# Optimization experiments

Measured on AMD Instinct MI355X. Metric: run time of the kernel, lower is better.

## Reference

```python
import jax, jax.numpy as jnp
import numpy as np

RADIUS = 2
K = 2 * RADIUS + 1          # kernel_size
NP = K ** 3                  # n_patches = 125
GAMMA_W = 3.3257199          # scipy.stats.t.ppf(1 - 0.005/2, df=8+8-2)
SIGMA_INV = jnp.array([0.1, 0.1, 0.1, 50., 50., 50., 10., 10., 10.], dtype=jnp.float32)


def _shift(x):
    """x: (C,H,W,T) -> (C, K^3, H, W, T): all neighbors within radius, zero-padded borders.
    Equivalent to Tile(pad=radius) + extract_patches_3ds(valid) + combine."""
    C, H, W, T = x.shape
    xp = jnp.pad(x, ((0, 0), (RADIUS, RADIUS), (RADIUS, RADIUS), (RADIUS, RADIUS)))
    sl = [xp[:, i:i + H, j:j + W, k:k + T]
          for i in range(K) for j in range(K) for k in range(K)]
    return jnp.stack(sl, axis=1)


def _compute_w(ei, ej, vi, vj):
    """Optimal weight w_ij (StatDenoiser.compute_w)."""
    d2 = (ei - ej) ** 2
    num = 2.0 * d2 + vi + vj
    den = 2.0 * (d2 + vi + vj)
    # den==0 implies num==0 (all terms nonneg) -> w = 0.5
    w = jnp.where(den == 0, 0.5, num / jnp.where(den == 0, 1.0, den))
    var_zero = (vi == 0) | (vj == 0)
    w = jnp.where(var_zero & (ei != ej), 1.0, w)
    return w


def _t_statistic(w):
    """t = sqrt(1/(2(1-w)) - 1), inf at w==1 (StatDenoiser.compute_t_statistic)."""
    w_safe = jnp.minimum(w, 1.0 - 1e-7)
    t = jnp.sqrt(jnp.maximum(1.0 / (2.0 * (1.0 - w_safe)) - 1.0, 0.0))
    return jnp.where(w >= 1.0, jnp.inf, t)


def setup_inputs() -> dict:
    key = jax.random.key(0)
    k1, k2, k3, k4 = jax.random.split(key, 4)
    noisy = jax.random.uniform(k1, (3, 128, 128, 4), dtype=jnp.float32)
    guidance = jax.random.normal(k2, (9, 128, 128, 4), dtype=jnp.float32)
    estimands = jax.random.uniform(k3, (3, 128, 128, 4), dtype=jnp.float32)
    estimands_variance = jax.random.uniform(k4, (3, 128, 128, 4), dtype=jnp.float32)
    return {"noisy": noisy, "guidance": guidance,
            "estimands": estimands, "estimands_variance": estimands_variance}


def reference(noisy, guidance, estimands, estimands_variance):
    # ---- bilateral weights from guidance (compute_bilateral_weights) ----
    sg = _shift(guidance)                                  # (9, P, H, W, T)
    diff2 = (sg - guidance[:, None]) ** 2                  # center patch == guidance itself
    bw = jnp.exp(-0.5 * jnp.einsum('c,cphwt->phwt', SIGMA_INV, diff2))  # (P,H,W,T)

    # ---- statistical membership (compute_membership) ----
    se = _shift(estimands)                                 # (3, P, H, W, T)
    sv = _shift(estimands_variance)
    ei = estimands[:, None]                                # center estimand
    vi = estimands_variance[:, None]
    w_ij = _compute_w(ei, se, vi, sv)                      # (3, P, H, W, T)
    t = _t_statistic(w_ij)
    membership = jnp.all(t <= GAMMA_W, axis=0).astype(noisy.dtype)      # (P,H,W,T)

    # ---- combine: normalized weighted average of neighbor radiance ----
    fw = bw * membership                                   # (P,H,W,T)
    sn = _shift(noisy)                                     # (3, P, H, W, T)
    out = jnp.einsum('phwt,cphwt->chwt', fw, sn) / jnp.maximum(fw.sum(axis=0), 1e-12)
    return out
```

## Files before the change

### kernel.cpp

```cpp
#include <hip/hip_runtime.h>

typedef float v2f __attribute__((ext_vector_type(2)));

namespace {

constexpr int H = 128, W = 128, NPIX = H * W;
constexpr double GAMMA_Wd = 3.3257199;
constexpr float GAM2 = (float)(GAMMA_Wd * GAMMA_Wd);
constexpr float VBIG  = 1e30f;
constexpr float NHUGE = -1e38f;

constexpr int TR = 4, TC = 16;
constexpr int HR = TR + 4, HC = TC + 4;
constexpr int NSITE = HR * HC;
constexpr int NK = 18;
constexpr int KP = 19;
constexpr int NTHR = 256;

constexpr double S2LOG2E = 1.2011224087864498;
constexpr float SCA0 = (float)(0.22360679774997896 * S2LOG2E);
constexpr float SCA1 = (float)(5.0                 * S2LOG2E);
constexpr float SCA2 = (float)(2.2360679774997896  * S2LOG2E);

__global__ __launch_bounds__(NTHR)
__attribute__((amdgpu_waves_per_eu(2, 8)))
void statden(const float4* __restrict__ noisy,
             const float4* __restrict__ guid,
             const float4* __restrict__ est,
             const float4* __restrict__ var,
             float4* __restrict__ out)
{
    __shared__ float4 halo[NSITE * KP];

    const int tid   = threadIdx.x;
    const int tiler = blockIdx.x >> 3;
    const int tilec = blockIdx.x & 7;
    const int r0 = tiler * TR - 2;
    const int c0 = tilec * TC - 2;

    for (int u = tid; u < NSITE * NK; u += NTHR) {
        const int k    = u / NSITE;
        const int site = u - k * NSITE;
        const int sr  = site / HC;
        const int scp = site - sr * HC;
        const int gr = r0 + sr;
        const int gc = c0 + scp;
        const bool varslot = (k >= 12) && (k < 15);
        float4 v;
        if (((unsigned)gr < (unsigned)H) && ((unsigned)gc < (unsigned)W)) {
            const int gpix = (gr << 7) + gc;
            if (k < 9) {
                const float sca = (k < 3) ? SCA0 : (k < 6) ? SCA1 : SCA2;
                const float4 g = guid[k * NPIX + gpix];
                v = make_float4(g.x * sca, g.y * sca, g.z * sca, g.w * sca);
            } else if (k < 12) {
                v = est[(k - 9) * NPIX + gpix];
            } else if (k < 15) {
                const float4 w4 = var[(k - 12) * NPIX + gpix];
                v.x = (w4.x == 0.f) ? -VBIG : GAM2 * w4.x;
                v.y = (w4.y == 0.f) ? -VBIG : GAM2 * w4.y;
                v.z = (w4.z == 0.f) ? -VBIG : GAM2 * w4.z;
                v.w = (w4.w == 0.f) ? -VBIG : GAM2 * w4.w;
            } else {
                v = noisy[(k - 15) * NPIX + gpix];
            }
        } else {
            const float pad = varslot ? -VBIG : 0.f;
            v = make_float4(pad, pad, pad, pad);
        }
        halo[site * KP + k] = v;
    }
    __syncthreads();

    const int p  = tid & 63;
    const int s  = tid >> 6;
    const int pr = p >> 4;
    const int pc = p & 15;

    const float4* cs = &halo[((pr + 2) * HC + (pc + 2)) * KP];

    v2f gcc[9][2];
    v2f nqc[2] = {{0.f, 0.f}, {0.f, 0.f}};
#pragma unroll
    for (int c = 0; c < 9; ++c) {
        const float4 g = cs[c];
        gcc[c][0] = (v2f){g.x, g.y};
        gcc[c][1] = (v2f){g.z, g.w};
        nqc[0] -= gcc[c][0] * gcc[c][0];
        nqc[1] -= gcc[c][1] * gcc[c][1];
    }
    v2f eiP[3][2], viP[3][2];
#pragma unroll
    for (int c = 0; c < 3; ++c) {
        const float4 e = cs[9 + c];
        eiP[c][0] = (v2f){e.x, e.y}; eiP[c][1] = (v2f){e.z, e.w};
        const float4 w4 = cs[12 + c];
        viP[c][0] = (v2f){w4.x, w4.y}; viP[c][1] = (v2f){w4.z, w4.w};
    }

    v2f accP[3][2] = {};
    v2f denP[2] = {};

#pragma unroll
    for (int cc = 0; cc < 7; ++cc) {
        const int col = (cc << 2) + s;
        if (col < 25) {
            const int di = col / 5 - 2;
            const int dj = col - (col / 5) * 5 - 2;
            const float4* js = &halo[((pr + 2 + di) * HC + (pc + 2 + dj)) * KP];

            v2f qj2[2] = {};
            v2f cr[4][2] = {};
#pragma unroll
            for (int c = 0; c < 9; ++c) {
                const float4 g = js[c];
                const v2f g01 = (v2f){g.x, g.y}, g23 = (v2f){g.z, g.w};
                qj2[0] += g01 * g01;  qj2[1] += g23 * g23;
                cr[0][0] += gcc[c][0] * g.x;  cr[0][1] += gcc[c][1] * g.x;
                cr[1][0] += gcc[c][0] * g.y;  cr[1][1] += gcc[c][1] * g.y;
                cr[2][0] += gcc[c][0] * g.z;  cr[2][1] += gcc[c][1] * g.z;
                cr[3][0] += gcc[c][0] * g.w;  cr[3][1] += gcc[c][1] * g.w;
            }

            v2f rm[4][2];
#pragma unroll
            for (int c = 0; c < 3; ++c) {
                const float4 e4 = js[9 + c];
                const float4 w4 = js[12 + c];
                const float ejs[4] = {e4.x, e4.y, e4.z, e4.w};
                const float vjs[4] = {w4.x, w4.y, w4.z, w4.w};
#pragma unroll
                for (int tt = 0; tt < 4; ++tt) {
#pragma unroll
                    for (int hf = 0; hf < 2; ++hf) {
                        const v2f d  = eiP[c][hf] - ejs[tt];
                        const v2f S  = viP[c][hf] + vjs[tt];
                        const v2f dd = d * d;
                        const v2f r  = S - dd;
                        const v2f z  = dd * NHUGE;
                        const v2f rf = __builtin_elementwise_max(r, z);
                        rm[tt][hf] = (c == 0) ? rf
                                   : __builtin_elementwise_min(rm[tt][hf], rf);
                    }
                }
            }

            v2f f01[4], f23[4];
#pragma unroll
            for (int tt = 0; tt < 4; ++tt) {
                const float qjt = qj2[tt >> 1][tt & 1];
                const v2f a0 = cr[tt][0] * 2.f + (nqc[0] - qjt);
                const v2f a1 = cr[tt][1] * 2.f + (nqc[1] - qjt);
                float fv[4];
#pragma unroll
                for (int t = 0; t < 4; ++t) {
                    const bool valid = (tt - t <= 2) && (t - tt <= 2);
                    if (valid) {
                        const float av = (t < 2) ? a0[t & 1] : a1[t & 1];
                        const float rv = (t < 2) ? rm[tt][0][t & 1] : rm[tt][1][t & 1];
                        const float e  = __builtin_exp2f(av);
                        fv[t] = (rv >= 0.f) ? e : 0.f;
                    } else {
                        fv[t] = 0.f;
                    }
                }
                f01[tt] = (v2f){fv[0], fv[1]};
                f23[tt] = (v2f){fv[2], fv[3]};
                denP[0] += f01[tt];
                denP[1] += f23[tt];
            }
#pragma unroll
            for (int c = 0; c < 3; ++c) {
                const float4 n4 = js[15 + c];
                const float njs[4] = {n4.x, n4.y, n4.z, n4.w};
#pragma unroll
                for (int tt = 0; tt < 4; ++tt) {
                    accP[c][0] += f01[tt] * njs[tt];
                    accP[c][1] += f23[tt] * njs[tt];
                }
            }
        }
    }

    __syncthreads();
    float* red = reinterpret_cast<float*>(halo);
    {
        float* r = red + (s * 64 + p) * 17;
#pragma unroll
        for (int c = 0; c < 3; ++c) {
            r[c * 4 + 0] = accP[c][0][0]; r[c * 4 + 1] = accP[c][0][1];
            r[c * 4 + 2] = accP[c][1][0]; r[c * 4 + 3] = accP[c][1][1];
        }
        r[12] = denP[0][0]; r[13] = denP[0][1];
        r[14] = denP[1][0]; r[15] = denP[1][1];
    }
    __syncthreads();

    if (tid < 64) {
        float v[16];
        const float* rp = red + p * 17;
#pragma unroll
        for (int i = 0; i < 16; ++i) v[i] = rp[i];
#pragma unroll
        for (int k = 1; k < 4; ++k) {
            const float* rk = red + (k * 64 + p) * 17;
#pragma unroll
            for (int i = 0; i < 16; ++i) v[i] += rk[i];
        }

        const float cnt[4] = {50.f, 25.f, 25.f, 50.f};
        const float qn[4]  = {nqc[0][0], nqc[0][1], nqc[1][0], nqc[1][1]};
        const float e0[4]  = {eiP[0][0][0], eiP[0][0][1], eiP[0][1][0], eiP[0][1][1]};
        const float e1[4]  = {eiP[1][0][0], eiP[1][0][1], eiP[1][1][0], eiP[1][1][1]};
        const float e2[4]  = {eiP[2][0][0], eiP[2][0][1], eiP[2][1][0], eiP[2][1][1]};
#pragma unroll
        for (int t = 0; t < 4; ++t) {
            const bool allz = (e0[t] == 0.f) && (e1[t] == 0.f) && (e2[t] == 0.f);
            const float f0 = allz ? __builtin_exp2f(qn[t]) : 0.f;
            v[12 + t] += cnt[t] * f0;
        }

#pragma unroll
        for (int t = 0; t < 4; ++t) {
            const float inv = 1.f / fmaxf(v[12 + t], 1e-12f);
            v[0 + t] *= inv; v[4 + t] *= inv; v[8 + t] *= inv;
        }
        const int pid = ((tiler * TR + pr) << 7) + tilec * TC + pc;
#pragma unroll
        for (int c = 0; c < 3; ++c) {
            float4 o;
            o.x = v[c * 4 + 0]; o.y = v[c * 4 + 1];
            o.z = v[c * 4 + 2]; o.w = v[c * 4 + 3];
            out[c * NPIX + pid] = o;
        }
    }
}

}

extern "C" void kernel_launch(void* const* d_in, const int* in_sizes, int n_in,
                              void* d_out, int out_size, void* d_ws, size_t ws_size,
                              hipStream_t stream)
{
    const float4* noisy = (const float4*)d_in[0];
    const float4* guid  = (const float4*)d_in[1];
    const float4* est   = (const float4*)d_in[2];
    const float4* var   = (const float4*)d_in[3];
    float4* out = (float4*)d_out;

    statden<<<(H / TR) * (W / TC), NTHR, 0, stream>>>(noisy, guid, est, var, out);
}
```

Before: 18.09 us.

## Split neighbor columns across eight wave slices and use dedicated reduction buffer

Doubles the block to 512 threads so each of 8 slices processes 3 of the 24 non-center neighbor columns, instead of 4 slices each looping over up to 7 columns. The center column is handled separately by the reducing threads after the cross-slice reduction. The reduction buffer moves to its own shared array, which removes the barrier that guarded reuse of the halo. The cost is more shared memory, a longer serial tail in the first wave, and possibly lower occupancy per block.

```diff
diff --git a/kernel.cpp b/kernel.cpp
--- a/kernel.cpp
+++ b/kernel.cpp
@@ -15,12 +15,91 @@
 constexpr int NSITE = HR * HC;
 constexpr int NK = 18;
 constexpr int KP = 19;
-constexpr int NTHR = 256;
+constexpr int NSL = 8;
+constexpr int NTHR = 64 * NSL;
 
 constexpr double S2LOG2E = 1.2011224087864498;
 constexpr float SCA0 = (float)(0.22360679774997896 * S2LOG2E);
 constexpr float SCA1 = (float)(5.0                 * S2LOG2E);
 constexpr float SCA2 = (float)(2.2360679774997896  * S2LOG2E);
+
+__device__ __forceinline__ void column_body(
+    const float4* __restrict__ js,
+    const v2f gcc[9][2], const v2f nqc[2],
+    const v2f eiP[3][2], const v2f viP[3][2],
+    v2f accP[3][2], v2f denP[2])
+{
+    v2f qj2[2] = {};
+    v2f cr[4][2] = {};
+#pragma unroll
+    for (int c = 0; c < 9; ++c) {
+        const float4 g = js[c];
+        const v2f g01 = (v2f){g.x, g.y}, g23 = (v2f){g.z, g.w};
+        qj2[0] += g01 * g01;  qj2[1] += g23 * g23;
+        cr[0][0] += gcc[c][0] * g.x;  cr[0][1] += gcc[c][1] * g.x;
+        cr[1][0] += gcc[c][0] * g.y;  cr[1][1] += gcc[c][1] * g.y;
+        cr[2][0] += gcc[c][0] * g.z;  cr[2][1] += gcc[c][1] * g.z;
+        cr[3][0] += gcc[c][0] * g.w;  cr[3][1] += gcc[c][1] * g.w;
+    }
+
+    v2f rm[4][2];
+#pragma unroll
+    for (int c = 0; c < 3; ++c) {
+        const float4 e4 = js[9 + c];
+        const float4 w4 = js[12 + c];
+        const float ejs[4] = {e4.x, e4.y, e4.z, e4.w};
+        const float vjs[4] = {w4.x, w4.y, w4.z, w4.w};
+#pragma unroll
+        for (int tt = 0; tt < 4; ++tt) {
+#pragma unroll
+            for (int hf = 0; hf < 2; ++hf) {
+                const v2f d  = eiP[c][hf] - ejs[tt];
+                const v2f S  = viP[c][hf] + vjs[tt];
+                const v2f dd = d * d;
+                const v2f r  = S - dd;
+                const v2f z  = dd * NHUGE;
+                const v2f rf = __builtin_elementwise_max(r, z);
+                rm[tt][hf] = (c == 0) ? rf
+                           : __builtin_elementwise_min(rm[tt][hf], rf);
+            }
+        }
+    }
+
+    v2f f01[4], f23[4];
+#pragma unroll
+    for (int tt = 0; tt < 4; ++tt) {
+        const float qjt = qj2[tt >> 1][tt & 1];
+        const v2f a0 = cr[tt][0] * 2.f + (nqc[0] - qjt);
+        const v2f a1 = cr[tt][1] * 2.f + (nqc[1] - qjt);
+        float fv[4];
+#pragma unroll
+        for (int t = 0; t < 4; ++t) {
+            const bool valid = (tt - t <= 2) && (t - tt <= 2);
+            if (valid) {
+                const float av = (t < 2) ? a0[t & 1] : a1[t & 1];
+                const float rv = (t < 2) ? rm[tt][0][t & 1] : rm[tt][1][t & 1];
+                const float e  = __builtin_exp2f(av);
+                fv[t] = (rv >= 0.f) ? e : 0.f;
+            } else {
+                fv[t] = 0.f;
+            }
+        }
+        f01[tt] = (v2f){fv[0], fv[1]};
+        f23[tt] = (v2f){fv[2], fv[3]};
+        denP[0] += f01[tt];
+        denP[1] += f23[tt];
+    }
+#pragma unroll
+    for (int c = 0; c < 3; ++c) {
+        const float4 n4 = js[15 + c];
+        const float njs[4] = {n4.x, n4.y, n4.z, n4.w};
+#pragma unroll
+        for (int tt = 0; tt < 4; ++tt) {
+            accP[c][0] += f01[tt] * njs[tt];
+            accP[c][1] += f23[tt] * njs[tt];
+        }
+    }
+}
 
 __global__ __launch_bounds__(NTHR)
 __attribute__((amdgpu_waves_per_eu(2, 8)))
@@ -31,6 +110,7 @@
              float4* __restrict__ out)
 {
     __shared__ float4 halo[NSITE * KP];
+    __shared__ float  red[NSL * 64 * 17];
 
     const int tid   = threadIdx.x;
     const int tiler = blockIdx.x >> 3;
@@ -102,88 +182,15 @@
     v2f denP[2] = {};
 
 #pragma unroll
-    for (int cc = 0; cc < 7; ++cc) {
-        const int col = (cc << 2) + s;
-        if (col < 25) {
-            const int di = col / 5 - 2;
-            const int dj = col - (col / 5) * 5 - 2;
-            const float4* js = &halo[((pr + 2 + di) * HC + (pc + 2 + dj)) * KP];
-
-            v2f qj2[2] = {};
-            v2f cr[4][2] = {};
-#pragma unroll
-            for (int c = 0; c < 9; ++c) {
-                const float4 g = js[c];
-                const v2f g01 = (v2f){g.x, g.y}, g23 = (v2f){g.z, g.w};
-                qj2[0] += g01 * g01;  qj2[1] += g23 * g23;
-                cr[0][0] += gcc[c][0] * g.x;  cr[0][1] += gcc[c][1] * g.x;
-                cr[1][0] += gcc[c][0] * g.y;  cr[1][1] += gcc[c][1] * g.y;
-                cr[2][0] += gcc[c][0] * g.z;  cr[2][1] += gcc[c][1] * g.z;
-                cr[3][0] += gcc[c][0] * g.w;  cr[3][1] += gcc[c][1] * g.w;
-            }
-
-            v2f rm[4][2];
-#pragma unroll
-            for (int c = 0; c < 3; ++c) {
-                const float4 e4 = js[9 + c];
-                const float4 w4 = js[12 + c];
-                const float ejs[4] = {e4.x, e4.y, e4.z, e4.w};
-                const float vjs[4] = {w4.x, w4.y, w4.z, w4.w};
-#pragma unroll
-                for (int tt = 0; tt < 4; ++tt) {
-#pragma unroll
-                    for (int hf = 0; hf < 2; ++hf) {
-                        const v2f d  = eiP[c][hf] - ejs[tt];
-                        const v2f S  = viP[c][hf] + vjs[tt];
-                        const v2f dd = d * d;
-                        const v2f r  = S - dd;
-                        const v2f z  = dd * NHUGE;
-                        const v2f rf = __builtin_elementwise_max(r, z);
-                        rm[tt][hf] = (c == 0) ? rf
-                                   : __builtin_elementwise_min(rm[tt][hf], rf);
-                    }
-                }
-            }
-
-            v2f f01[4], f23[4];
-#pragma unroll
-            for (int tt = 0; tt < 4; ++tt) {
-                const float qjt = qj2[tt >> 1][tt & 1];
-                const v2f a0 = cr[tt][0] * 2.f + (nqc[0] - qjt);
-                const v2f a1 = cr[tt][1] * 2.f + (nqc[1] - qjt);
-                float fv[4];
-#pragma unroll
-                for (int t = 0; t < 4; ++t) {
-                    const bool valid = (tt - t <= 2) && (t - tt <= 2);
-                    if (valid) {
-                        const float av = (t < 2) ? a0[t & 1] : a1[t & 1];
-                        const float rv = (t < 2) ? rm[tt][0][t & 1] : rm[tt][1][t & 1];
-                        const float e  = __builtin_exp2f(av);
-                        fv[t] = (rv >= 0.f) ? e : 0.f;
-                    } else {
-                        fv[t] = 0.f;
-                    }
-                }
-                f01[tt] = (v2f){fv[0], fv[1]};
-                f23[tt] = (v2f){fv[2], fv[3]};
-                denP[0] += f01[tt];
-                denP[1] += f23[tt];
-            }
-#pragma unroll
-            for (int c = 0; c < 3; ++c) {
-                const float4 n4 = js[15 + c];
-                const float njs[4] = {n4.x, n4.y, n4.z, n4.w};
-#pragma unroll
-                for (int tt = 0; tt < 4; ++tt) {
-                    accP[c][0] += f01[tt] * njs[tt];
-                    accP[c][1] += f23[tt] * njs[tt];
-                }
-            }
-        }
-    }
-
-    __syncthreads();
-    float* red = reinterpret_cast<float*>(halo);
+    for (int mm = 0; mm < 3; ++mm) {
+        const int m   = s * 3 + mm;
+        const int col = m + (m >= 12 ? 1 : 0);
+        const int di  = col / 5 - 2;
+        const int dj  = col - (col / 5) * 5 - 2;
+        const float4* js = &halo[((pr + 2 + di) * HC + (pc + 2 + dj)) * KP];
+        column_body(js, gcc, nqc, eiP, viP, accP, denP);
+    }
+
     {
         float* r = red + (s * 64 + p) * 17;
 #pragma unroll
@@ -202,10 +209,23 @@
 #pragma unroll
         for (int i = 0; i < 16; ++i) v[i] = rp[i];
 #pragma unroll
-        for (int k = 1; k < 4; ++k) {
+        for (int k = 1; k < NSL; ++k) {
             const float* rk = red + (k * 64 + p) * 17;
 #pragma unroll
             for (int i = 0; i < 16; ++i) v[i] += rk[i];
+        }
+
+        {
+            v2f accC[3][2] = {};
+            v2f denC[2] = {};
+            column_body(cs, gcc, nqc, eiP, viP, accC, denC);
+#pragma unroll
+            for (int c = 0; c < 3; ++c) {
+                v[c * 4 + 0] += accC[c][0][0]; v[c * 4 + 1] += accC[c][0][1];
+                v[c * 4 + 2] += accC[c][1][0]; v[c * 4 + 3] += accC[c][1][1];
+            }
+            v[12] += denC[0][0]; v[13] += denC[0][1];
+            v[14] += denC[1][0]; v[15] += denC[1][1];
         }
 
         const float cnt[4] = {50.f, 25.f, 25.f, 50.f};
```

New measurement: 16.62 us. 1.09x faster.
